# Kernel tuning notes

Hardware: AMD Instinct MI355X
Metric: run time of the kernel (lower is better)

## Reference

```python
import jax, jax.numpy as jnp
from jax import lax
import numpy as np

B, S, D, H, O = 16384, 128, 512, 1024, 10


def setup_inputs() -> dict:
    key = jax.random.key(0)
    ks = jax.random.split(key, 7)
    def lin(kw, kb, out_d, in_d):
        bound = 1.0 / np.sqrt(in_d)
        w = jax.random.uniform(kw, (out_d, in_d), jnp.float32, -bound, bound)
        b = jax.random.uniform(kb, (out_d,), jnp.float32, -bound, bound)
        return w, b
    x = jax.random.normal(ks[0], (B, D), jnp.float32)
    Whx_w, Whx_b = lin(ks[1], ks[2], H, D)
    Whh_w, Whh_b = lin(ks[3], ks[4], H, H)
    Wph_w, Wph_b = lin(ks[5], ks[6], O, H)
    return {"x": x, "Whx_w": Whx_w, "Whx_b": Whx_b, "Whh_w": Whh_w,
            "Whh_b": Whh_b, "Wph_w": Wph_w, "Wph_b": Wph_b, "seq_length": S}


def reference(x, Whx_w, Whx_b, Whh_w, Whh_b, Wph_w, Wph_b, seq_length):
    # The original forward feeds the SAME x at every timestep, so the
    # input projection W_hx(x) is a loop-invariant we compute once.
    xW = x @ Whx_w.T + Whx_b  # [B, H]

    def step(h, _):
        h = jnp.tanh(xW + h @ Whh_w.T + Whh_b)
        return h, None

    h0 = jnp.zeros((x.shape[0], Whh_w.shape[0]), x.dtype)  # h starts at 0
    h, _ = lax.scan(step, h0, None, length=seq_length)
    out = h @ Wph_w.T + Wph_b  # [B, O]
    return jax.nn.softmax(out, axis=-1)
```

## Files before the change

### kernel.cpp

```cpp
#include <hip/hip_runtime.h>

#define BATCH    16384
#define H_DIM    1024
#define D_DIM    512
#define O_DIM    10
#define SEQ      128
#define BM       64
#define NTHREADS 1024
#define HSTR     1040
#define QW       (127.0f / 0.03125f)
#define QSCALE   (0.03125f / (127.0f * 127.0f))

typedef __bf16 bf16;
typedef __bf16 bf16x8 __attribute__((ext_vector_type(8)));
typedef float  f32x16 __attribute__((ext_vector_type(16)));
typedef float  f32x4  __attribute__((ext_vector_type(4)));
typedef int    i32x4  __attribute__((ext_vector_type(4)));
typedef int    i32x16 __attribute__((ext_vector_type(16)));

__device__ bf16        g_x[BATCH * D_DIM];
__device__ bf16        g_whx[H_DIM * D_DIM];
__device__ signed char g_whhq[H_DIM * H_DIM];
__device__ bf16        g_wph[O_DIM * H_DIM];
__device__ bf16        g_xwp[BATCH * H_DIM];
__device__ float       g_bias[H_DIM];
__device__ float       g_bph[O_DIM];

__device__ __forceinline__ float fast_tanh(float z) {
  float e = __expf(2.0f * z);
  return 1.0f - 2.0f / (e + 1.0f);
}

__global__ void cvt_bf16(const float* __restrict__ src, bf16* __restrict__ dst, int n) {
  const int i = (blockIdx.x * blockDim.x + threadIdx.x) * 8;
  if (i >= n) return;
  f32x4 s0 = *(const f32x4*)(src + i);
  f32x4 s1 = *(const f32x4*)(src + i + 4);
  bf16x8 v;
  #pragma unroll
  for (int j = 0; j < 4; ++j) { v[j] = (bf16)s0[j]; v[4 + j] = (bf16)s1[j]; }
  *(bf16x8*)(dst + i) = v;
}

__global__ void pack_whhq(const float* __restrict__ src, signed char* __restrict__ dst) {
  const int t = blockIdx.x * blockDim.x + threadIdx.x;
  const int lane = t & 63;
  const int nt   = (t >> 6) & 1;
  const int kc   = (t >> 7) & 31;
  const int w    = t >> 12;
  const int row = w * 64 + nt * 32 + (lane & 31);
  const int col = kc * 32 + (lane >> 5) * 16;
  const float* s = src + (size_t)row * H_DIM + col;
  #pragma unroll
  for (int j = 0; j < 16; ++j) {
    int q = (int)lrintf(s[j] * QW);
    q = q > 127 ? 127 : (q < -127 ? -127 : q);
    dst[(size_t)t * 16 + j] = (signed char)q;
  }
}

__global__ void cvt_bias(const float* __restrict__ bx, const float* __restrict__ bh,
                         const float* __restrict__ bp) {
  const int i = blockIdx.x * blockDim.x + threadIdx.x;
  if (i < H_DIM) g_bias[i] = bx[i] + bh[i];
  if (i < O_DIM) g_bph[i]  = bp[i];
}

#define MFMA4_BF16(A0, A1, B)                                                            \
  accf[0][0] = __builtin_amdgcn_mfma_f32_32x32x16_bf16(A0, (B)[0], accf[0][0], 0, 0, 0); \
  accf[0][1] = __builtin_amdgcn_mfma_f32_32x32x16_bf16(A0, (B)[1], accf[0][1], 0, 0, 0); \
  accf[1][0] = __builtin_amdgcn_mfma_f32_32x32x16_bf16(A1, (B)[0], accf[1][0], 0, 0, 0); \
  accf[1][1] = __builtin_amdgcn_mfma_f32_32x32x16_bf16(A1, (B)[1], accf[1][1], 0, 0, 0);

#define MFMA4_I8(A0, A1, B)                                                              \
  acc[0][0] = __builtin_amdgcn_mfma_i32_32x32x32_i8(A0, (B)[0], acc[0][0], 0, 0, 0);     \
  acc[0][1] = __builtin_amdgcn_mfma_i32_32x32x32_i8(A0, (B)[1], acc[0][1], 0, 0, 0);     \
  acc[1][0] = __builtin_amdgcn_mfma_i32_32x32x32_i8(A1, (B)[0], acc[1][0], 0, 0, 0);     \
  acc[1][1] = __builtin_amdgcn_mfma_i32_32x32x32_i8(A1, (B)[1], acc[1][1], 0, 0, 0);

__global__ __launch_bounds__(NTHREADS, 3)
void rnn_fused(float* __restrict__ out)
{
  extern __shared__ char smem[];
  signed char* hbuf = (signed char*)smem;

  const int tid  = threadIdx.x;
  const int wave = tid >> 6;
  const int lane = tid & 63;
  const int m31  = lane & 31;
  const int q    = lane >> 5;
  const int r0   = blockIdx.x * BM;
  const int nw0  = wave * 64;

  const signed char* bstr = g_whhq + (size_t)wave * (32 * 2 * 1024) + lane * 16;
  bf16* xbase = g_xwp + ((size_t)blockIdx.x * 16 + wave) * 4096 + lane * 8;

  {
    f32x16 accf[2][2];
    #pragma unroll
    for (int mt = 0; mt < 2; ++mt)
      #pragma unroll
      for (int nt = 0; nt < 2; ++nt)
        #pragma unroll
        for (int i = 0; i < 16; ++i) accf[mt][nt][i] = 0.0f;

    const bf16* aBase = g_x + (size_t)(r0 + m31) * D_DIM + q * 8;
    #pragma unroll 4
    for (int kc = 0; kc < D_DIM / 16; ++kc) {
      bf16x8 a0 = *(const bf16x8*)(aBase + kc * 16);
      bf16x8 a1 = *(const bf16x8*)(aBase + (size_t)32 * D_DIM + kc * 16);
      bf16x8 b[2];
      #pragma unroll
      for (int nt = 0; nt < 2; ++nt)
        b[nt] = *(const bf16x8*)(g_whx + (size_t)(nw0 + nt * 32 + m31) * D_DIM + kc * 16 + q * 8);
      MFMA4_BF16(a0, a1, b);
    }

    bf16x8 xq[8];
    #pragma unroll
    for (int nt = 0; nt < 2; ++nt) {
      const int col = nw0 + nt * 32 + m31;
      const float bias = g_bias[col];
      #pragma unroll
      for (int mt = 0; mt < 2; ++mt)
        #pragma unroll
        for (int r = 0; r < 16; ++r) {
          const int row = mt * 32 + (r & 3) + 8 * (r >> 2) + 4 * q;
          const int idx = (nt * 2 + mt) * 16 + r;
          const float v = accf[mt][nt][r] + bias;
          xq[idx >> 3][idx & 7] = (bf16)v;
          hbuf[row * HSTR + col] = (signed char)__float2int_rn(fast_tanh(v) * 127.0f);
        }
    }
    #pragma unroll
    for (int i = 0; i < 8; ++i)
      __builtin_nontemporal_store(xq[i], (bf16x8*)(xbase + i * 512));
  }
  __syncthreads();

  const signed char* aP0 = hbuf + m31 * HSTR + q * 16;
  const signed char* aP1 = aP0 + 32 * HSTR;

  for (int step = 1; step < SEQ; ++step) {
    i32x16 acc[2][2];
    #pragma unroll
    for (int mt = 0; mt < 2; ++mt)
      #pragma unroll
      for (int nt = 0; nt < 2; ++nt)
        #pragma unroll
        for (int i = 0; i < 16; ++i) acc[mt][nt][i] = 0;

    i32x4 bq[4][2];
    #pragma unroll
    for (int p = 0; p < 4; ++p)
      #pragma unroll
      for (int nt = 0; nt < 2; ++nt)
        bq[p][nt] = *(const i32x4*)(bstr + ((p * 2 + nt) * 1024));

    #pragma unroll
    for (int kc = 0; kc < 32; ++kc) {
      i32x4 a0 = *(const i32x4*)(aP0 + kc * 32);
      i32x4 a1 = *(const i32x4*)(aP1 + kc * 32);
      MFMA4_I8(a0, a1, bq[kc & 3]);
      if (kc + 4 < 32) {
        #pragma unroll
        for (int nt = 0; nt < 2; ++nt)
          bq[kc & 3][nt] = *(const i32x4*)(bstr + (((kc + 4) * 2 + nt) * 1024));
      }
    }

    bf16x8 xq[8];
    #pragma unroll
    for (int i = 0; i < 8; ++i)
      xq[i] = __builtin_nontemporal_load((const bf16x8*)(xbase + i * 512));

    __syncthreads();

    #pragma unroll
    for (int nt = 0; nt < 2; ++nt) {
      const int col = nw0 + nt * 32 + m31;
      #pragma unroll
      for (int mt = 0; mt < 2; ++mt)
        #pragma unroll
        for (int r = 0; r < 16; ++r) {
          const int row = mt * 32 + (r & 3) + 8 * (r >> 2) + 4 * q;
          const int idx = (nt * 2 + mt) * 16 + r;
          const float v = (float)acc[mt][nt][r] * QSCALE + (float)xq[idx >> 3][idx & 7];
          hbuf[row * HSTR + col] = (signed char)__float2int_rn(fast_tanh(v) * 127.0f);
        }
    }
    __syncthreads();
  }

  {
    const int row  = tid >> 4;
    const int tsub = tid & 15;
    float p[O_DIM];
    #pragma unroll
    for (int o = 0; o < O_DIM; ++o) p[o] = 0.0f;

    const signed char* hrow = hbuf + row * HSTR + tsub * 64;
    for (int kk = 0; kk < 64; kk += 16) {
      i32x4 hp = *(const i32x4*)(hrow + kk);
      float hf[16];
      #pragma unroll
      for (int d = 0; d < 4; ++d)
        #pragma unroll
        for (int j = 0; j < 4; ++j)
          hf[d * 4 + j] = (float)((int)(hp[d] << ((3 - j) * 8)) >> 24);
      #pragma unroll
      for (int o = 0; o < O_DIM; ++o) {
        bf16x8 wv0 = *(const bf16x8*)(g_wph + (size_t)o * H_DIM + tsub * 64 + kk);
        bf16x8 wv1 = *(const bf16x8*)(g_wph + (size_t)o * H_DIM + tsub * 64 + kk + 8);
        #pragma unroll
        for (int j = 0; j < 8; ++j) {
          p[o] += hf[j] * (float)wv0[j];
          p[o] += hf[8 + j] * (float)wv1[j];
        }
      }
    }
    #pragma unroll
    for (int d = 1; d < 16; d <<= 1)
      #pragma unroll
      for (int o = 0; o < O_DIM; ++o) p[o] += __shfl_xor(p[o], d, 16);

    if (tsub == 0) {
      float v[O_DIM], mx = -1e30f;
      #pragma unroll
      for (int o = 0; o < O_DIM; ++o) {
        v[o] = p[o] * (1.0f / 127.0f) + g_bph[o];
        mx = fmaxf(mx, v[o]);
      }
      float s = 0.0f;
      #pragma unroll
      for (int o = 0; o < O_DIM; ++o) { v[o] = __expf(v[o] - mx); s += v[o]; }
      const float inv = 1.0f / s;
      #pragma unroll
      for (int o = 0; o < O_DIM; ++o)
        out[(size_t)(r0 + row) * O_DIM + o] = v[o] * inv;
    }
  }
}

extern "C" void kernel_launch(void* const* d_in, const int* in_sizes, int n_in,
                              void* d_out, int out_size, void* d_ws, size_t ws_size,
                              hipStream_t stream)
{
  (void)d_ws; (void)ws_size; (void)in_sizes; (void)n_in; (void)out_size;
  const float* x     = (const float*)d_in[0];
  const float* Whx_w = (const float*)d_in[1];
  const float* Whx_b = (const float*)d_in[2];
  const float* Whh_w = (const float*)d_in[3];
  const float* Whh_b = (const float*)d_in[4];
  const float* Wph_w = (const float*)d_in[5];
  const float* Wph_b = (const float*)d_in[6];
  float* out = (float*)d_out;

  (void)hipFuncSetAttribute((const void*)rnn_fused,
                            hipFuncAttributeMaxDynamicSharedMemorySize, BM * HSTR);

  bf16* gx; bf16* gwhx; signed char* gwhhq; bf16* gwph;
  hipGetSymbolAddress((void**)&gx,    HIP_SYMBOL(g_x));
  hipGetSymbolAddress((void**)&gwhx,  HIP_SYMBOL(g_whx));
  hipGetSymbolAddress((void**)&gwhhq, HIP_SYMBOL(g_whhq));
  hipGetSymbolAddress((void**)&gwph,  HIP_SYMBOL(g_wph));

  cvt_bf16<<<BATCH * D_DIM / 2048, 256, 0, stream>>>(x,     gx,   BATCH * D_DIM);
  cvt_bf16<<<H_DIM * D_DIM / 2048, 256, 0, stream>>>(Whx_w, gwhx, H_DIM * D_DIM);
  pack_whhq<<<65536 / 256, 256, 0, stream>>>(Whh_w, gwhhq);
  cvt_bf16<<<(O_DIM * H_DIM / 8 + 255) / 256, 256, 0, stream>>>(Wph_w, gwph, O_DIM * H_DIM);
  cvt_bias<<<4, 256, 0, stream>>>(Whx_b, Whh_b, Wph_b);

  const dim3 grid(BATCH / BM), block(NTHREADS);
  const size_t lds = (size_t)BM * HSTR;
  rnn_fused<<<grid, block, lds, stream>>>(out);
}
```

Before: 4.599 ms.

## Double-buffer hidden state in LDS, keep xW in registers, split N tiles

Replaces the single hidden-state LDS buffer with ping-pong buffers, which removes one __syncthreads per timestep. The input projection xW now stays in registers across all steps, so the global scratch array and its per-step reloads go away. The 2x2 MFMA tiles are split into two sequential half-N passes to hold fewer live accumulators. Launch bounds are raised to 4 blocks per CU, although the doubled LDS (about 133KB per block) may not allow that occupancy.

Result: slower. 4.889 ms (+6.3%).

```diff
diff --git a/kernel.cpp b/kernel.cpp
--- a/kernel.cpp
+++ b/kernel.cpp
@@ -8,6 +8,7 @@
 #define BM       64
 #define NTHREADS 1024
 #define HSTR     1040
+#define HBUF_SZ  (BM * HSTR)
 #define QW       (127.0f / 0.03125f)
 #define QSCALE   (0.03125f / (127.0f * 127.0f))
 
@@ -22,7 +23,6 @@
 __device__ bf16        g_whx[H_DIM * D_DIM];
 __device__ signed char g_whhq[H_DIM * H_DIM];
 __device__ bf16        g_wph[O_DIM * H_DIM];
-__device__ bf16        g_xwp[BATCH * H_DIM];
 __device__ float       g_bias[H_DIM];
 __device__ float       g_bph[O_DIM];
 
@@ -66,23 +66,31 @@
   if (i < O_DIM) g_bph[i]  = bp[i];
 }
 
-#define MFMA4_BF16(A0, A1, B)                                                            \
-  accf[0][0] = __builtin_amdgcn_mfma_f32_32x32x16_bf16(A0, (B)[0], accf[0][0], 0, 0, 0); \
-  accf[0][1] = __builtin_amdgcn_mfma_f32_32x32x16_bf16(A0, (B)[1], accf[0][1], 0, 0, 0); \
-  accf[1][0] = __builtin_amdgcn_mfma_f32_32x32x16_bf16(A1, (B)[0], accf[1][0], 0, 0, 0); \
-  accf[1][1] = __builtin_amdgcn_mfma_f32_32x32x16_bf16(A1, (B)[1], accf[1][1], 0, 0, 0);
-
-#define MFMA4_I8(A0, A1, B)                                                              \
-  acc[0][0] = __builtin_amdgcn_mfma_i32_32x32x32_i8(A0, (B)[0], acc[0][0], 0, 0, 0);     \
-  acc[0][1] = __builtin_amdgcn_mfma_i32_32x32x32_i8(A0, (B)[1], acc[0][1], 0, 0, 0);     \
-  acc[1][0] = __builtin_amdgcn_mfma_i32_32x32x32_i8(A1, (B)[0], acc[1][0], 0, 0, 0);     \
-  acc[1][1] = __builtin_amdgcn_mfma_i32_32x32x32_i8(A1, (B)[1], acc[1][1], 0, 0, 0);
-
-__global__ __launch_bounds__(NTHREADS, 3)
+#define P0_EPI(ACC, MT)                                                                   \
+  _Pragma("unroll")                                                                       \
+  for (int r = 0; r < 16; ++r) {                                                          \
+    const int row = (MT) * 32 + (r & 3) + 8 * (r >> 2) + 4 * q;                           \
+    const int idx = (hh * 2 + (MT)) * 16 + r;                                             \
+    const float v = (ACC)[r] + bias;                                                      \
+    xq[idx >> 3][idx & 7] = (bf16)v;                                                      \
+    hcur[row * HSTR + col] = (signed char)__float2int_rn(fast_tanh(v) * 127.0f);          \
+  }
+
+#define ST_EPI(ACC, MT)                                                                   \
+  _Pragma("unroll")                                                                       \
+  for (int r = 0; r < 16; ++r) {                                                          \
+    const int row = (MT) * 32 + (r & 3) + 8 * (r >> 2) + 4 * q;                           \
+    const int idx = (hh * 2 + (MT)) * 16 + r;                                             \
+    const float v = (float)(ACC)[r] * QSCALE + (float)xq[idx >> 3][idx & 7];              \
+    hnxt[row * HSTR + col] = (signed char)__float2int_rn(fast_tanh(v) * 127.0f);          \
+  }
+
+__global__ __launch_bounds__(NTHREADS, 4)
 void rnn_fused(float* __restrict__ out)
 {
   extern __shared__ char smem[];
-  signed char* hbuf = (signed char*)smem;
+  signed char* hcur = (signed char*)smem;
+  signed char* hnxt = (signed char*)smem + HBUF_SZ;
 
   const int tid  = threadIdx.x;
   const int wave = tid >> 6;
@@ -93,103 +101,69 @@
   const int nw0  = wave * 64;
 
   const signed char* bstr = g_whhq + (size_t)wave * (32 * 2 * 1024) + lane * 16;
-  bf16* xbase = g_xwp + ((size_t)blockIdx.x * 16 + wave) * 4096 + lane * 8;
+
+  bf16x8 xq[8];
 
   {
-    f32x16 accf[2][2];
-    #pragma unroll
-    for (int mt = 0; mt < 2; ++mt)
-      #pragma unroll
-      for (int nt = 0; nt < 2; ++nt)
-        #pragma unroll
-        for (int i = 0; i < 16; ++i) accf[mt][nt][i] = 0.0f;
-
     const bf16* aBase = g_x + (size_t)(r0 + m31) * D_DIM + q * 8;
-    #pragma unroll 4
-    for (int kc = 0; kc < D_DIM / 16; ++kc) {
-      bf16x8 a0 = *(const bf16x8*)(aBase + kc * 16);
-      bf16x8 a1 = *(const bf16x8*)(aBase + (size_t)32 * D_DIM + kc * 16);
-      bf16x8 b[2];
-      #pragma unroll
-      for (int nt = 0; nt < 2; ++nt)
-        b[nt] = *(const bf16x8*)(g_whx + (size_t)(nw0 + nt * 32 + m31) * D_DIM + kc * 16 + q * 8);
-      MFMA4_BF16(a0, a1, b);
-    }
-
-    bf16x8 xq[8];
-    #pragma unroll
-    for (int nt = 0; nt < 2; ++nt) {
-      const int col = nw0 + nt * 32 + m31;
+    #pragma unroll
+    for (int hh = 0; hh < 2; ++hh) {
+      f32x16 accf0, accf1;
+      #pragma unroll
+      for (int i = 0; i < 16; ++i) { accf0[i] = 0.0f; accf1[i] = 0.0f; }
+
+      const bf16* bBase = g_whx + (size_t)(nw0 + hh * 32 + m31) * D_DIM + q * 8;
+      #pragma unroll 4
+      for (int kc = 0; kc < D_DIM / 16; ++kc) {
+        bf16x8 a0 = *(const bf16x8*)(aBase + kc * 16);
+        bf16x8 a1 = *(const bf16x8*)(aBase + (size_t)32 * D_DIM + kc * 16);
+        bf16x8 b  = *(const bf16x8*)(bBase + kc * 16);
+        accf0 = __builtin_amdgcn_mfma_f32_32x32x16_bf16(a0, b, accf0, 0, 0, 0);
+        accf1 = __builtin_amdgcn_mfma_f32_32x32x16_bf16(a1, b, accf1, 0, 0, 0);
+      }
+
+      const int col = nw0 + hh * 32 + m31;
       const float bias = g_bias[col];
-      #pragma unroll
-      for (int mt = 0; mt < 2; ++mt)
-        #pragma unroll
-        for (int r = 0; r < 16; ++r) {
-          const int row = mt * 32 + (r & 3) + 8 * (r >> 2) + 4 * q;
-          const int idx = (nt * 2 + mt) * 16 + r;
-          const float v = accf[mt][nt][r] + bias;
-          xq[idx >> 3][idx & 7] = (bf16)v;
-          hbuf[row * HSTR + col] = (signed char)__float2int_rn(fast_tanh(v) * 127.0f);
-        }
-    }
-    #pragma unroll
-    for (int i = 0; i < 8; ++i)
-      __builtin_nontemporal_store(xq[i], (bf16x8*)(xbase + i * 512));
+      P0_EPI(accf0, 0)
+      P0_EPI(accf1, 1)
+    }
   }
   __syncthreads();
 
-  const signed char* aP0 = hbuf + m31 * HSTR + q * 16;
-  const signed char* aP1 = aP0 + 32 * HSTR;
+  const int aoff = m31 * HSTR + q * 16;
 
   for (int step = 1; step < SEQ; ++step) {
-    i32x16 acc[2][2];
-    #pragma unroll
-    for (int mt = 0; mt < 2; ++mt)
-      #pragma unroll
-      for (int nt = 0; nt < 2; ++nt)
-        #pragma unroll
-        for (int i = 0; i < 16; ++i) acc[mt][nt][i] = 0;
-
-    i32x4 bq[4][2];
-    #pragma unroll
-    for (int p = 0; p < 4; ++p)
-      #pragma unroll
-      for (int nt = 0; nt < 2; ++nt)
-        bq[p][nt] = *(const i32x4*)(bstr + ((p * 2 + nt) * 1024));
-
-    #pragma unroll
-    for (int kc = 0; kc < 32; ++kc) {
-      i32x4 a0 = *(const i32x4*)(aP0 + kc * 32);
-      i32x4 a1 = *(const i32x4*)(aP1 + kc * 32);
-      MFMA4_I8(a0, a1, bq[kc & 3]);
-      if (kc + 4 < 32) {
-        #pragma unroll
-        for (int nt = 0; nt < 2; ++nt)
-          bq[kc & 3][nt] = *(const i32x4*)(bstr + (((kc + 4) * 2 + nt) * 1024));
-      }
-    }
-
-    bf16x8 xq[8];
-    #pragma unroll
-    for (int i = 0; i < 8; ++i)
-      xq[i] = __builtin_nontemporal_load((const bf16x8*)(xbase + i * 512));
+    #pragma unroll
+    for (int hh = 0; hh < 2; ++hh) {
+      i32x16 acc0, acc1;
+      #pragma unroll
+      for (int i = 0; i < 16; ++i) { acc0[i] = 0; acc1[i] = 0; }
+
+      i32x4 bq[4];
+      #pragma unroll
+      for (int p = 0; p < 4; ++p)
+        bq[p] = *(const i32x4*)(bstr + (p * 2 + hh) * 1024);
+
+      const signed char* aP0 = hcur + aoff;
+      const signed char* aP1 = aP0 + 32 * HSTR;
+
+      #pragma unroll
+      for (int kc = 0; kc < 32; ++kc) {
+        i32x4 a0 = *(const i32x4*)(aP0 + kc * 32);
+        i32x4 a1 = *(const i32x4*)(aP1 + kc * 32);
+        acc0 = __builtin_amdgcn_mfma_i32_32x32x32_i8(a0, bq[kc & 3], acc0, 0, 0, 0);
+        acc1 = __builtin_amdgcn_mfma_i32_32x32x32_i8(a1, bq[kc & 3], acc1, 0, 0, 0);
+        if (kc + 4 < 32)
+          bq[kc & 3] = *(const i32x4*)(bstr + ((kc + 4) * 2 + hh) * 1024);
+      }
+
+      const int col = nw0 + hh * 32 + m31;
+      ST_EPI(acc0, 0)
+      ST_EPI(acc1, 1)
+    }
 
     __syncthreads();
-
-    #pragma unroll
-    for (int nt = 0; nt < 2; ++nt) {
-      const int col = nw0 + nt * 32 + m31;
-      #pragma unroll
-      for (int mt = 0; mt < 2; ++mt)
-        #pragma unroll
-        for (int r = 0; r < 16; ++r) {
-          const int row = mt * 32 + (r & 3) + 8 * (r >> 2) + 4 * q;
-          const int idx = (nt * 2 + mt) * 16 + r;
-          const float v = (float)acc[mt][nt][r] * QSCALE + (float)xq[idx >> 3][idx & 7];
-          hbuf[row * HSTR + col] = (signed char)__float2int_rn(fast_tanh(v) * 127.0f);
-        }
-    }
-    __syncthreads();
+    signed char* t = hcur; hcur = hnxt; hnxt = t;
   }
 
   {
@@ -199,7 +173,7 @@
     #pragma unroll
     for (int o = 0; o < O_DIM; ++o) p[o] = 0.0f;
 
-    const signed char* hrow = hbuf + row * HSTR + tsub * 64;
+    const signed char* hrow = hcur + row * HSTR + tsub * 64;
     for (int kk = 0; kk < 64; kk += 16) {
       i32x4 hp = *(const i32x4*)(hrow + kk);
       float hf[16];
@@ -257,7 +231,7 @@
   float* out = (float*)d_out;
 
   (void)hipFuncSetAttribute((const void*)rnn_fused,
-                            hipFuncAttributeMaxDynamicSharedMemorySize, BM * HSTR);
+                            hipFuncAttributeMaxDynamicSharedMemorySize, 2 * HBUF_SZ);
 
   bf16* gx; bf16* gwhx; signed char* gwhhq; bf16* gwph;
   hipGetSymbolAddress((void**)&gx,    HIP_SYMBOL(g_x));
@@ -272,6 +246,6 @@
   cvt_bias<<<4, 256, 0, stream>>>(Whx_b, Whh_b, Wph_b);
 
   const dim3 grid(BATCH / BM), block(NTHREADS);
-  const size_t lds = (size_t)BM * HSTR;
+  const size_t lds = 2 * HBUF_SZ;
   rnn_fused<<<grid, block, lds, stream>>>(out);
 }
```

## Widen per-wave N tile to 128 and keep projected input in registers

Applied to the files above, without the earlier changes.

Halves the block to 8 waves, each owning 128 output columns (4 N-tiles) instead of 64, and repacks Whh int8 weights to match. The bf16 input projection stays in registers for all timesteps instead of a global scratch round trip. The K loop is restructured with even/odd double-buffered A/B fragments and rolling weight prefetch across steps, and it uses lighter LDS barriers. This raises register pressure and cuts waves per block, which may limit latency hiding and occupancy.

After: 9.594 ms. +108.6%, slower.

```diff
diff --git a/kernel.cpp b/kernel.cpp
--- a/kernel.cpp
+++ b/kernel.cpp
@@ -6,8 +6,9 @@
 #define O_DIM    10
 #define SEQ      128
 #define BM       64
-#define NTHREADS 1024
+#define NTHREADS 512
 #define HSTR     1040
+#define HBUF_SZ  (BM * HSTR)
 #define QW       (127.0f / 0.03125f)
 #define QSCALE   (0.03125f / (127.0f * 127.0f))
 
@@ -22,7 +23,6 @@
 __device__ bf16        g_whx[H_DIM * D_DIM];
 __device__ signed char g_whhq[H_DIM * H_DIM];
 __device__ bf16        g_wph[O_DIM * H_DIM];
-__device__ bf16        g_xwp[BATCH * H_DIM];
 __device__ float       g_bias[H_DIM];
 __device__ float       g_bph[O_DIM];
 
@@ -45,10 +45,10 @@
 __global__ void pack_whhq(const float* __restrict__ src, signed char* __restrict__ dst) {
   const int t = blockIdx.x * blockDim.x + threadIdx.x;
   const int lane = t & 63;
-  const int nt   = (t >> 6) & 1;
-  const int kc   = (t >> 7) & 31;
-  const int w    = t >> 12;
-  const int row = w * 64 + nt * 32 + (lane & 31);
+  const int nt   = (t >> 6) & 3;
+  const int kc   = (t >> 8) & 31;
+  const int w    = t >> 13;
+  const int row = w * 128 + nt * 32 + (lane & 31);
   const int col = kc * 32 + (lane >> 5) * 16;
   const float* s = src + (size_t)row * H_DIM + col;
   #pragma unroll
@@ -66,19 +66,12 @@
   if (i < O_DIM) g_bph[i]  = bp[i];
 }
 
-#define MFMA4_BF16(A0, A1, B)                                                            \
-  accf[0][0] = __builtin_amdgcn_mfma_f32_32x32x16_bf16(A0, (B)[0], accf[0][0], 0, 0, 0); \
-  accf[0][1] = __builtin_amdgcn_mfma_f32_32x32x16_bf16(A0, (B)[1], accf[0][1], 0, 0, 0); \
-  accf[1][0] = __builtin_amdgcn_mfma_f32_32x32x16_bf16(A1, (B)[0], accf[1][0], 0, 0, 0); \
-  accf[1][1] = __builtin_amdgcn_mfma_f32_32x32x16_bf16(A1, (B)[1], accf[1][1], 0, 0, 0);
-
-#define MFMA4_I8(A0, A1, B)                                                              \
-  acc[0][0] = __builtin_amdgcn_mfma_i32_32x32x32_i8(A0, (B)[0], acc[0][0], 0, 0, 0);     \
-  acc[0][1] = __builtin_amdgcn_mfma_i32_32x32x32_i8(A0, (B)[1], acc[0][1], 0, 0, 0);     \
-  acc[1][0] = __builtin_amdgcn_mfma_i32_32x32x32_i8(A1, (B)[0], acc[1][0], 0, 0, 0);     \
-  acc[1][1] = __builtin_amdgcn_mfma_i32_32x32x32_i8(A1, (B)[1], acc[1][1], 0, 0, 0);
-
-__global__ __launch_bounds__(NTHREADS, 3)
+#define LDS_BARRIER()                                      \
+  asm volatile("s_waitcnt lgkmcnt(0)" ::: "memory");       \
+  __builtin_amdgcn_s_barrier();                            \
+  asm volatile("" ::: "memory");
+
+__global__ __launch_bounds__(NTHREADS, 2)
 void rnn_fused(float* __restrict__ out)
 {
   extern __shared__ char smem[];
@@ -90,17 +83,18 @@
   const int m31  = lane & 31;
   const int q    = lane >> 5;
   const int r0   = blockIdx.x * BM;
-  const int nw0  = wave * 64;
-
-  const signed char* bstr = g_whhq + (size_t)wave * (32 * 2 * 1024) + lane * 16;
-  bf16* xbase = g_xwp + ((size_t)blockIdx.x * 16 + wave) * 4096 + lane * 8;
+  const int nw0  = wave * 128;
+
+  const signed char* bstr = g_whhq + (size_t)wave * 131072 + lane * 16;
+
+  bf16x8 xq[16];
 
   {
-    f32x16 accf[2][2];
+    f32x16 accf[2][4];
     #pragma unroll
     for (int mt = 0; mt < 2; ++mt)
       #pragma unroll
-      for (int nt = 0; nt < 2; ++nt)
+      for (int nt = 0; nt < 4; ++nt)
         #pragma unroll
         for (int i = 0; i < 16; ++i) accf[mt][nt][i] = 0.0f;
 
@@ -109,16 +103,16 @@
     for (int kc = 0; kc < D_DIM / 16; ++kc) {
       bf16x8 a0 = *(const bf16x8*)(aBase + kc * 16);
       bf16x8 a1 = *(const bf16x8*)(aBase + (size_t)32 * D_DIM + kc * 16);
-      bf16x8 b[2];
-      #pragma unroll
-      for (int nt = 0; nt < 2; ++nt)
-        b[nt] = *(const bf16x8*)(g_whx + (size_t)(nw0 + nt * 32 + m31) * D_DIM + kc * 16 + q * 8);
-      MFMA4_BF16(a0, a1, b);
-    }
-
-    bf16x8 xq[8];
-    #pragma unroll
-    for (int nt = 0; nt < 2; ++nt) {
+      #pragma unroll
+      for (int nt = 0; nt < 4; ++nt) {
+        bf16x8 b = *(const bf16x8*)(g_whx + (size_t)(nw0 + nt * 32 + m31) * D_DIM + kc * 16 + q * 8);
+        accf[0][nt] = __builtin_amdgcn_mfma_f32_32x32x16_bf16(a0, b, accf[0][nt], 0, 0, 0);
+        accf[1][nt] = __builtin_amdgcn_mfma_f32_32x32x16_bf16(a1, b, accf[1][nt], 0, 0, 0);
+      }
+    }
+
+    #pragma unroll
+    for (int nt = 0; nt < 4; ++nt) {
       const int col = nw0 + nt * 32 + m31;
       const float bias = g_bias[col];
       #pragma unroll
@@ -132,52 +126,64 @@
           hbuf[row * HSTR + col] = (signed char)__float2int_rn(fast_tanh(v) * 127.0f);
         }
     }
-    #pragma unroll
-    for (int i = 0; i < 8; ++i)
-      __builtin_nontemporal_store(xq[i], (bf16x8*)(xbase + i * 512));
-  }
-  __syncthreads();
-
-  const signed char* aP0 = hbuf + m31 * HSTR + q * 16;
-  const signed char* aP1 = aP0 + 32 * HSTR;
+  }
+
+  i32x4 bqE[4], bqO[4];
+  #pragma unroll
+  for (int nt = 0; nt < 4; ++nt) bqE[nt] = *(const i32x4*)(bstr + (0 * 4 + nt) * 1024);
+  #pragma unroll
+  for (int nt = 0; nt < 4; ++nt) bqO[nt] = *(const i32x4*)(bstr + (1 * 4 + nt) * 1024);
+
+  LDS_BARRIER()
+
+  const int aoff = m31 * HSTR + q * 16;
 
   for (int step = 1; step < SEQ; ++step) {
-    i32x16 acc[2][2];
+    i32x16 acc[2][4];
     #pragma unroll
     for (int mt = 0; mt < 2; ++mt)
       #pragma unroll
-      for (int nt = 0; nt < 2; ++nt)
+      for (int nt = 0; nt < 4; ++nt)
         #pragma unroll
         for (int i = 0; i < 16; ++i) acc[mt][nt][i] = 0;
 
-    i32x4 bq[4][2];
-    #pragma unroll
-    for (int p = 0; p < 4; ++p)
-      #pragma unroll
-      for (int nt = 0; nt < 2; ++nt)
-        bq[p][nt] = *(const i32x4*)(bstr + ((p * 2 + nt) * 1024));
-
-    #pragma unroll
-    for (int kc = 0; kc < 32; ++kc) {
-      i32x4 a0 = *(const i32x4*)(aP0 + kc * 32);
-      i32x4 a1 = *(const i32x4*)(aP1 + kc * 32);
-      MFMA4_I8(a0, a1, bq[kc & 3]);
-      if (kc + 4 < 32) {
-        #pragma unroll
-        for (int nt = 0; nt < 2; ++nt)
-          bq[kc & 3][nt] = *(const i32x4*)(bstr + (((kc + 4) * 2 + nt) * 1024));
-      }
-    }
-
-    bf16x8 xq[8];
-    #pragma unroll
-    for (int i = 0; i < 8; ++i)
-      xq[i] = __builtin_nontemporal_load((const bf16x8*)(xbase + i * 512));
-
-    __syncthreads();
-
-    #pragma unroll
-    for (int nt = 0; nt < 2; ++nt) {
+    const signed char* aP0 = hbuf + aoff;
+    const signed char* aP1 = aP0 + 32 * HSTR;
+
+    i32x4 aE0 = *(const i32x4*)(aP0);
+    i32x4 aE1 = *(const i32x4*)(aP1);
+
+    #pragma unroll
+    for (int t = 0; t < 16; ++t) {
+      i32x4 aO0 = *(const i32x4*)(aP0 + (2 * t + 1) * 32);
+      i32x4 aO1 = *(const i32x4*)(aP1 + (2 * t + 1) * 32);
+      #pragma unroll
+      for (int nt = 0; nt < 4; ++nt) {
+        acc[0][nt] = __builtin_amdgcn_mfma_i32_32x32x32_i8(aE0, bqE[nt], acc[0][nt], 0, 0, 0);
+        acc[1][nt] = __builtin_amdgcn_mfma_i32_32x32x32_i8(aE1, bqE[nt], acc[1][nt], 0, 0, 0);
+      }
+      #pragma unroll
+      for (int nt = 0; nt < 4; ++nt)
+        bqE[nt] = *(const i32x4*)(bstr + ((((2 * t + 2) & 31) * 4) + nt) * 1024);
+
+      if (t < 15) {
+        aE0 = *(const i32x4*)(aP0 + (2 * t + 2) * 32);
+        aE1 = *(const i32x4*)(aP1 + (2 * t + 2) * 32);
+      }
+      #pragma unroll
+      for (int nt = 0; nt < 4; ++nt) {
+        acc[0][nt] = __builtin_amdgcn_mfma_i32_32x32x32_i8(aO0, bqO[nt], acc[0][nt], 0, 0, 0);
+        acc[1][nt] = __builtin_amdgcn_mfma_i32_32x32x32_i8(aO1, bqO[nt], acc[1][nt], 0, 0, 0);
+      }
+      #pragma unroll
+      for (int nt = 0; nt < 4; ++nt)
+        bqO[nt] = *(const i32x4*)(bstr + ((((2 * t + 3) & 31) * 4) + nt) * 1024);
+    }
+
+    LDS_BARRIER()
+
+    #pragma unroll
+    for (int nt = 0; nt < 4; ++nt) {
       const int col = nw0 + nt * 32 + m31;
       #pragma unroll
       for (int mt = 0; mt < 2; ++mt)
@@ -189,18 +195,19 @@
           hbuf[row * HSTR + col] = (signed char)__float2int_rn(fast_tanh(v) * 127.0f);
         }
     }
-    __syncthreads();
+
+    LDS_BARRIER()
   }
 
   {
-    const int row  = tid >> 4;
-    const int tsub = tid & 15;
+    const int row  = tid >> 3;
+    const int tsub = tid & 7;
     float p[O_DIM];
     #pragma unroll
     for (int o = 0; o < O_DIM; ++o) p[o] = 0.0f;
 
-    const signed char* hrow = hbuf + row * HSTR + tsub * 64;
-    for (int kk = 0; kk < 64; kk += 16) {
+    const signed char* hrow = hbuf + row * HSTR + tsub * 128;
+    for (int kk = 0; kk < 128; kk += 16) {
       i32x4 hp = *(const i32x4*)(hrow + kk);
       float hf[16];
       #pragma unroll
@@ -210,8 +217,8 @@
           hf[d * 4 + j] = (float)((int)(hp[d] << ((3 - j) * 8)) >> 24);
       #pragma unroll
       for (int o = 0; o < O_DIM; ++o) {
-        bf16x8 wv0 = *(const bf16x8*)(g_wph + (size_t)o * H_DIM + tsub * 64 + kk);
-        bf16x8 wv1 = *(const bf16x8*)(g_wph + (size_t)o * H_DIM + tsub * 64 + kk + 8);
+        bf16x8 wv0 = *(const bf16x8*)(g_wph + (size_t)o * H_DIM + tsub * 128 + kk);
+        bf16x8 wv1 = *(const bf16x8*)(g_wph + (size_t)o * H_DIM + tsub * 128 + kk + 8);
         #pragma unroll
         for (int j = 0; j < 8; ++j) {
           p[o] += hf[j] * (float)wv0[j];
@@ -220,9 +227,9 @@
       }
     }
     #pragma unroll
-    for (int d = 1; d < 16; d <<= 1)
-      #pragma unroll
-      for (int o = 0; o < O_DIM; ++o) p[o] += __shfl_xor(p[o], d, 16);
+    for (int d = 1; d < 8; d <<= 1)
+      #pragma unroll
+      for (int o = 0; o < O_DIM; ++o) p[o] += __shfl_xor(p[o], d, 8);
 
     if (tsub == 0) {
       float v[O_DIM], mx = -1e30f;
@@ -257,7 +264,7 @@
   float* out = (float*)d_out;
 
   (void)hipFuncSetAttribute((const void*)rnn_fused,
-                            hipFuncAttributeMaxDynamicSharedMemorySize, BM * HSTR);
+                            hipFuncAttributeMaxDynamicSharedMemorySize, HBUF_SZ);
 
   bf16* gx; bf16* gwhx; signed char* gwhhq; bf16* gwph;
   hipGetSymbolAddress((void**)&gx,    HIP_SYMBOL(g_x));
@@ -272,6 +279,5 @@
   cvt_bias<<<4, 256, 0, stream>>>(Whx_b, Whh_b, Wph_b);
 
   const dim3 grid(BATCH / BM), block(NTHREADS);
-  const size_t lds = (size_t)BM * HSTR;
-  rnn_fused<<<grid, block, lds, stream>>>(out);
-}
+  rnn_fused<<<grid, block, HBUF_SZ, stream>>>(out);
+}
```

## Double-buffer hidden state in LDS and prefetch weights across timesteps

Applied to the files above, without the earlier changes.

Splits the int8 hidden-state buffer into current and next LDS halves, so each timestep needs one barrier instead of two. The Whh weight prefetch ring now wraps across step boundaries, so the next step's first weight fragments load during the current step's epilogue. MFMA priority is raised around the inner loop. LDS per block doubles, which may cut the number of resident blocks per CU and reduce latency hiding.

Result: no change. 4.615 ms (+0.4%).

```diff
diff --git a/kernel.cpp b/kernel.cpp
--- a/kernel.cpp
+++ b/kernel.cpp
@@ -8,6 +8,7 @@
 #define BM       64
 #define NTHREADS 1024
 #define HSTR     1040
+#define HBUF_SZ  (BM * HSTR)
 #define QW       (127.0f / 0.03125f)
 #define QSCALE   (0.03125f / (127.0f * 127.0f))
 
@@ -78,11 +79,17 @@
   acc[1][0] = __builtin_amdgcn_mfma_i32_32x32x32_i8(A1, (B)[0], acc[1][0], 0, 0, 0);     \
   acc[1][1] = __builtin_amdgcn_mfma_i32_32x32x32_i8(A1, (B)[1], acc[1][1], 0, 0, 0);
 
+#define LDS_BARRIER()                                      \
+  asm volatile("s_waitcnt lgkmcnt(0)" ::: "memory");       \
+  __builtin_amdgcn_s_barrier();                            \
+  asm volatile("" ::: "memory");
+
 __global__ __launch_bounds__(NTHREADS, 3)
 void rnn_fused(float* __restrict__ out)
 {
   extern __shared__ char smem[];
-  signed char* hbuf = (signed char*)smem;
+  signed char* hcur = (signed char*)smem;
+  signed char* hnxt = (signed char*)smem + HBUF_SZ;
 
   const int tid  = threadIdx.x;
   const int wave = tid >> 6;
@@ -95,6 +102,8 @@
   const signed char* bstr = g_whhq + (size_t)wave * (32 * 2 * 1024) + lane * 16;
   bf16* xbase = g_xwp + ((size_t)blockIdx.x * 16 + wave) * 4096 + lane * 8;
 
+  i32x4 bq[4][2];
+
   {
     f32x16 accf[2][2];
     #pragma unroll
@@ -129,17 +138,25 @@
           const int idx = (nt * 2 + mt) * 16 + r;
           const float v = accf[mt][nt][r] + bias;
           xq[idx >> 3][idx & 7] = (bf16)v;
-          hbuf[row * HSTR + col] = (signed char)__float2int_rn(fast_tanh(v) * 127.0f);
+          hcur[row * HSTR + col] = (signed char)__float2int_rn(fast_tanh(v) * 127.0f);
         }
     }
     #pragma unroll
     for (int i = 0; i < 8; ++i)
       __builtin_nontemporal_store(xq[i], (bf16x8*)(xbase + i * 512));
   }
-  __syncthreads();
-
-  const signed char* aP0 = hbuf + m31 * HSTR + q * 16;
-  const signed char* aP1 = aP0 + 32 * HSTR;
+
+  asm volatile("s_waitcnt vmcnt(0)" ::: "memory");
+
+  #pragma unroll
+  for (int p = 0; p < 4; ++p)
+    #pragma unroll
+    for (int nt = 0; nt < 2; ++nt)
+      bq[p][nt] = *(const i32x4*)(bstr + (p * 2 + nt) * 1024);
+
+  LDS_BARRIER()
+
+  const int aoff = m31 * HSTR + q * 16;
 
   for (int step = 1; step < SEQ; ++step) {
     i32x16 acc[2][2];
@@ -150,31 +167,25 @@
         #pragma unroll
         for (int i = 0; i < 16; ++i) acc[mt][nt][i] = 0;
 
-    i32x4 bq[4][2];
-    #pragma unroll
-    for (int p = 0; p < 4; ++p)
-      #pragma unroll
-      for (int nt = 0; nt < 2; ++nt)
-        bq[p][nt] = *(const i32x4*)(bstr + ((p * 2 + nt) * 1024));
-
+    const signed char* aP0 = hcur + aoff;
+    const signed char* aP1 = aP0 + 32 * HSTR;
+
+    __builtin_amdgcn_s_setprio(1);
     #pragma unroll
     for (int kc = 0; kc < 32; ++kc) {
       i32x4 a0 = *(const i32x4*)(aP0 + kc * 32);
       i32x4 a1 = *(const i32x4*)(aP1 + kc * 32);
       MFMA4_I8(a0, a1, bq[kc & 3]);
-      if (kc + 4 < 32) {
-        #pragma unroll
-        for (int nt = 0; nt < 2; ++nt)
-          bq[kc & 3][nt] = *(const i32x4*)(bstr + (((kc + 4) * 2 + nt) * 1024));
-      }
-    }
+      #pragma unroll
+      for (int nt = 0; nt < 2; ++nt)
+        bq[kc & 3][nt] = *(const i32x4*)(bstr + ((((kc + 4) & 31) * 2 + nt) * 1024));
+    }
+    __builtin_amdgcn_s_setprio(0);
 
     bf16x8 xq[8];
     #pragma unroll
     for (int i = 0; i < 8; ++i)
       xq[i] = __builtin_nontemporal_load((const bf16x8*)(xbase + i * 512));
-
-    __syncthreads();
 
     #pragma unroll
     for (int nt = 0; nt < 2; ++nt) {
@@ -186,10 +197,12 @@
           const int row = mt * 32 + (r & 3) + 8 * (r >> 2) + 4 * q;
           const int idx = (nt * 2 + mt) * 16 + r;
           const float v = (float)acc[mt][nt][r] * QSCALE + (float)xq[idx >> 3][idx & 7];
-          hbuf[row * HSTR + col] = (signed char)__float2int_rn(fast_tanh(v) * 127.0f);
+          hnxt[row * HSTR + col] = (signed char)__float2int_rn(fast_tanh(v) * 127.0f);
         }
     }
-    __syncthreads();
+
+    LDS_BARRIER()
+    signed char* t = hcur; hcur = hnxt; hnxt = t;
   }
 
   {
@@ -199,7 +212,7 @@
     #pragma unroll
     for (int o = 0; o < O_DIM; ++o) p[o] = 0.0f;
 
-    const signed char* hrow = hbuf + row * HSTR + tsub * 64;
+    const signed char* hrow = hcur + row * HSTR + tsub * 64;
     for (int kk = 0; kk < 64; kk += 16) {
       i32x4 hp = *(const i32x4*)(hrow + kk);
       float hf[16];
@@ -257,7 +270,7 @@
   float* out = (float*)d_out;
 
   (void)hipFuncSetAttribute((const void*)rnn_fused,
-                            hipFuncAttributeMaxDynamicSharedMemorySize, BM * HSTR);
+                            hipFuncAttributeMaxDynamicSharedMemorySize, 2 * HBUF_SZ);
 
   bf16* gx; bf16* gwhx; signed char* gwhhq; bf16* gwph;
   hipGetSymbolAddress((void**)&gx,    HIP_SYMBOL(g_x));
@@ -272,6 +285,6 @@
   cvt_bias<<<4, 256, 0, stream>>>(Whx_b, Whh_b, Wph_b);
 
   const dim3 grid(BATCH / BM), block(NTHREADS);
-  const size_t lds = (size_t)BM * HSTR;
+  const size_t lds = 2 * HBUF_SZ;
   rnn_fused<<<grid, block, lds, stream>>>(out);
 }
```
